# Performance work log

Measured on AMD Instinct MI355X. Metric: run time of the kernel, lower is better.

## Reference

```python
import jax, jax.numpy as jnp
import numpy as np

DIM = 1024
NUM_HEADS = 16
HEAD_DIM = DIM // NUM_HEADS


def setup_inputs() -> dict:
    key = jax.random.key(0)
    k1, k2, k3 = jax.random.split(key, 3)
    x = jax.random.normal(k1, (2, 2048, DIM), dtype=jnp.float32)
    # nn.Linear weights stored as [out, in]; apply as x @ W.T
    w_qkv = jax.random.normal(k2, (3 * DIM, DIM), dtype=jnp.float32) * (1.0 / np.sqrt(DIM))
    w_out = jax.random.normal(k3, (DIM, DIM), dtype=jnp.float32) * (1.0 / np.sqrt(DIM))
    return {"x": x, "w_qkv": w_qkv, "w_out": w_out}


def reference(x, w_qkv, w_out):
    b, t, _ = x.shape
    qkv = x @ w_qkv.T                                  # [b, t, 3*dim]
    qkv = qkv.reshape(b, t, 3, NUM_HEADS, HEAD_DIM)    # (three h d) split order
    q, k, v = jnp.moveaxis(qkv, 2, 0)                  # each [b, t, h, d]
    q = q.transpose(0, 2, 1, 3)                        # [b, h, t, d]
    k = k.transpose(0, 2, 1, 3)
    v = v.transpose(0, 2, 1, 3)
    attn = jnp.einsum('bhid,bhjd->bhij', q, k) / np.sqrt(HEAD_DIM)
    causal_mask = jnp.triu(jnp.ones((t, t), dtype=bool), k=1)
    attn = jnp.where(causal_mask, -jnp.inf, attn)
    attn = jax.nn.softmax(attn, axis=-1)
    out = jnp.einsum('bhij,bhjd->bhid', attn, v)
    out = out.transpose(0, 2, 1, 3).reshape(b, t, DIM)
    return out @ w_out.T
```

## Files before the change

kernel.cpp:

```cpp
#include <hip/hip_runtime.h>

#define DIM_ 1024
#define HEADS_ 16
#define HD_ 64
#define T_ 2048
#define BATCH_ 2
#define QKVN_ 3072

typedef unsigned short u16;
typedef unsigned int u32;
typedef float f32x4 __attribute__((ext_vector_type(4)));
typedef float f32x16 __attribute__((ext_vector_type(16)));
typedef short s16x8 __attribute__((ext_vector_type(8)));
typedef unsigned short u16x4 __attribute__((ext_vector_type(4)));

__device__ __forceinline__ u16 f2bf(float f) {
  unsigned u = __float_as_uint(f);
  u += 0x7fffu + ((u >> 16) & 1u);
  return (u16)(u >> 16);
}

__device__ __forceinline__ float fexp2(float x) {
  float r;
  asm("v_exp_f32 %0, %1" : "=v"(r) : "v"(x));
  return r;
}

__device__ __forceinline__ u32 cvtpk(float a, float b) {
  u32 r;
  asm("v_cvt_pk_bf16_f32 %0, %1, %2" : "=v"(r) : "v"(a), "v"(b));
  return r;
}

__global__ __launch_bounds__(256) void cvt_all(const float* __restrict__ x,
                                               const float* __restrict__ wqkv,
                                               const float* __restrict__ wout,
                                               u16* __restrict__ outbase) {
  int i = blockIdx.x * 256 + threadIdx.x;
  const float4* src;
  int off;
  if (i < 1048576) { src = (const float4*)x; off = i; }
  else if (i < 1835008) { src = (const float4*)wqkv; off = i - 1048576; }
  else { src = (const float4*)wout; off = i - 1835008; }
  float4 v = src[off];
  u16x4 o;
  o.x = f2bf(v.x); o.y = f2bf(v.y); o.z = f2bf(v.z); o.w = f2bf(v.w);
  reinterpret_cast<u16x4*>(outbase)[i] = o;
}

__device__ __forceinline__ void gld_lds16(const void* g, void* l) {
  auto gp = (__attribute__((address_space(1))) char*)(unsigned long long)g;
  auto lp = (__attribute__((address_space(3))) char*)(unsigned int)(unsigned long long)l;
  __builtin_amdgcn_global_load_lds(gp, lp, 16, 0, 0);
}

template <int MODE>
__global__ __launch_bounds__(256) void gemm1(const u16* __restrict__ A,
                                             const u16* __restrict__ B,
                                             void* __restrict__ Cv,
                                             u16* __restrict__ vto) {
  constexpr int K = 1024;
  constexpr int NN = (MODE == 1) ? 1024 : QKVN_;
  __shared__ __align__(16) u16 smem[(MODE == 2) ? 8704 : 8192];
  u16* As = smem;
  u16* Bs = smem + 4096;
  const int nt = blockIdx.x, mt = blockIdx.y;
  const int tid = threadIdx.x;
  const int lane = tid & 63;
  const int w = tid >> 6;
  const int wr = w >> 1, wc = w & 1;
  const int lrow = lane & 15, kg = lane >> 4;
  const u16* Ag = A + (size_t)(mt * 128) * K;
  const u16* Bg = B + (size_t)(nt * 128) * K;

  f32x4 acc[4][4];
#pragma unroll
  for (int i = 0; i < 4; ++i)
#pragma unroll
    for (int j = 0; j < 4; ++j) {
      f32x4 z = {0.f, 0.f, 0.f, 0.f};
      acc[i][j] = z;
    }

  const int e0 = tid * 8;
  const int row0 = e0 >> 5, kc0 = e0 & 31;
  const int row1 = row0 + 64, kc1 = kc0;
  const int ldsoff0 = (tid & ~63) * 16;
  const int ldsoff1 = (256 + (tid & ~63)) * 16;

  for (int k0 = 0; k0 < K; k0 += 32) {
    gld_lds16(Ag + (size_t)row0 * K + k0 + kc0, (char*)As + ldsoff0);
    gld_lds16(Ag + (size_t)row1 * K + k0 + kc1, (char*)As + ldsoff1);
    gld_lds16(Bg + (size_t)row0 * K + k0 + kc0, (char*)Bs + ldsoff0);
    gld_lds16(Bg + (size_t)row1 * K + k0 + kc1, (char*)Bs + ldsoff1);
    __syncthreads();
    s16x8 a[4], b[4];
#pragma unroll
    for (int mf = 0; mf < 4; ++mf)
      a[mf] = *(const s16x8*)&As[(wr * 64 + mf * 16 + lrow) * 32 + 8 * kg];
#pragma unroll
    for (int nf = 0; nf < 4; ++nf)
      b[nf] = *(const s16x8*)&Bs[(wc * 64 + nf * 16 + lrow) * 32 + 8 * kg];
#pragma unroll
    for (int mf = 0; mf < 4; ++mf)
#pragma unroll
      for (int nf = 0; nf < 4; ++nf)
        acc[mf][nf] = __builtin_amdgcn_mfma_f32_16x16x32_bf16(a[mf], b[nf], acc[mf][nf], 0, 0, 0);
    __syncthreads();
  }

  if (MODE == 1) {
    float* C = (float*)Cv;
#pragma unroll
    for (int mf = 0; mf < 4; ++mf)
#pragma unroll
      for (int nf = 0; nf < 4; ++nf)
#pragma unroll
        for (int j = 0; j < 4; ++j) {
          int r = mt * 128 + wr * 64 + mf * 16 + 4 * kg + j;
          int c = nt * 128 + wc * 64 + nf * 16 + lrow;
          C[(size_t)r * NN + c] = acc[mf][nf][j];
        }
  } else if (nt < 16) {
    u16* qkvo = (u16*)Cv;
#pragma unroll
    for (int mf = 0; mf < 4; ++mf)
#pragma unroll
      for (int nf = 0; nf < 4; ++nf)
#pragma unroll
        for (int j = 0; j < 4; ++j) {
          int r = mt * 128 + wr * 64 + mf * 16 + 4 * kg + j;
          int c = nt * 128 + wc * 64 + nf * 16 + lrow;
          qkvo[(size_t)r * QKVN_ + c] = f2bf(acc[mf][nf][j]);
        }
  } else {
    const int c16 = tid >> 4, chunk = tid & 15;
    const int bb = mt >> 4;
    const int tb = (mt & 15) * 128 + chunk * 8;
#pragma unroll
    for (int p = 0; p < 2; ++p) {
      __syncthreads();
      if (wc == p) {
#pragma unroll
        for (int mf = 0; mf < 4; ++mf)
#pragma unroll
          for (int nf = 0; nf < 4; ++nf) {
            const int cl = nf * 16 + lrow;
            const int rl = wr * 64 + mf * 16 + 4 * kg;
            u16x4 pk;
            pk.x = f2bf(acc[mf][nf][0]); pk.y = f2bf(acc[mf][nf][1]);
            pk.z = f2bf(acc[mf][nf][2]); pk.w = f2bf(acc[mf][nf][3]);
            *(u16x4*)&smem[cl * 136 + rl] = pk;
          }
      }
      __syncthreads();
#pragma unroll
      for (int pp = 0; pp < 4; ++pp) {
        const int cl = pp * 16 + c16;
        const int cg = nt * 128 + p * 64 + cl;
        const int hV = (cg >> 6) & 15, d = cg & 63;
        const s16x8 v = *(const s16x8*)&smem[cl * 136 + chunk * 8];
        *(s16x8*)(vto + ((size_t)((bb * 16 + hV) * 64 + d)) * T_ + tb) = v;
      }
    }
  }
}

__global__ __launch_bounds__(256, 2) void attn_fwd(const u16* __restrict__ qkv,
                                                   const u16* __restrict__ vt,
                                                   u16* __restrict__ o) {
  const int gid = blockIdx.x;
  const int pr = gid >> 5;
  const int bh = gid & 31;
  const int b = bh >> 4, h = bh & 15;
  const int tid = threadIdx.x;
  const int lane = tid & 63;
  const int qw = (tid >> 6) & 1;
  const int kvg = tid >> 7;
  const int l31 = lane & 31, hi = lane >> 5;

  __shared__ __align__(16) char smem[65536];

  const int row_s = tid >> 3, slot_s = tid & 7;
  const u16* Kbase = qkv + (size_t)(b * T_) * QKVN_ + 1024 + h * 64;
  const u16* Vbase = vt + (size_t)(bh * 64) * T_;
  const u16* KgA = Kbase + (size_t)row_s * QKVN_ + slot_s * 8;
  const u16* KgB = KgA + (size_t)32 * QKVN_;
  const u16* VgA = Vbase + (size_t)row_s * T_ + slot_s * 8;
  const u16* VgB = VgA + (size_t)32 * T_;
  const int dstA = row_s * 128 + ((slot_s ^ (row_s & 7)) << 4);

  const int rbyte = l31 * 128;
  const int xsw = l31 & 7;
  const float CEXP = 0.18033688011112042f;

  for (int ph = 0; ph < 2; ++ph) {
    const int jt = (ph == 0) ? (31 - pr) : pr;
    const int nt = jt + 1;
    const int nrt = (nt + 1) >> 1;
    const int qrow0 = 64 * jt + 32 * qw;

    s16x8 qf[4];
    {
      const u16* qp = qkv + (size_t)(b * T_ + qrow0 + l31) * QKVN_ + h * 64 + 8 * hi;
#pragma unroll
      for (int ksl = 0; ksl < 4; ++ksl)
        qf[ksl] = *(const s16x8*)(qp + 16 * ksl);
    }

    f32x16 o0v, o1v;
#pragma unroll
    for (int r = 0; r < 16; ++r) { o0v[r] = 0.f; o1v[r] = 0.f; }
    float mrun = -__builtin_inff(), lrun = 0.0f;

    __syncthreads();
    *(s16x8*)(smem + dstA)                 = *(const s16x8*)KgA;
    *(s16x8*)(smem + 4096 + dstA)          = *(const s16x8*)KgB;
    *(s16x8*)(smem + 32768 + dstA)         = *(const s16x8*)VgA;
    *(s16x8*)(smem + 32768 + 4096 + dstA)  = *(const s16x8*)VgB;
    if (nt > 1) {
      *(s16x8*)(smem + 8192 + dstA)                = *(const s16x8*)(KgA + (size_t)64 * QKVN_);
      *(s16x8*)(smem + 8192 + 4096 + dstA)         = *(const s16x8*)(KgB + (size_t)64 * QKVN_);
      *(s16x8*)(smem + 32768 + 8192 + dstA)        = *(const s16x8*)(VgA + 64);
      *(s16x8*)(smem + 32768 + 8192 + 4096 + dstA) = *(const s16x8*)(VgB + 64);
    }

    int cur = 0;
    for (int r = 0; r < nrt; ++r) {
      const int t = 2 * r + kvg;
      const bool pe = (2 * r + 2 < nt), po = (2 * r + 3 < nt);
      s16x8 ke0, ke1, ve0, ve1, ko0, ko1, vo0, vo1;
      if (pe) {
        const size_t kofs = (size_t)(2 * r + 2) * 64 * QKVN_;
        const int vofs = (2 * r + 2) * 64;
        ke0 = *(const s16x8*)(KgA + kofs);
        ke1 = *(const s16x8*)(KgB + kofs);
        ve0 = *(const s16x8*)(VgA + vofs);
        ve1 = *(const s16x8*)(VgB + vofs);
      }
      if (po) {
        const size_t kofs = (size_t)(2 * r + 3) * 64 * QKVN_;
        const int vofs = (2 * r + 3) * 64;
        ko0 = *(const s16x8*)(KgA + kofs);
        ko1 = *(const s16x8*)(KgB + kofs);
        vo0 = *(const s16x8*)(VgA + vofs);
        vo1 = *(const s16x8*)(VgB + vofs);
      }
      __syncthreads();

      if (t < nt) {
        const char* Kc = smem + cur * 16384 + kvg * 8192;
        const char* Vc = smem + 32768 + cur * 16384 + kvg * 8192;
        const bool isdiag = (t == nt - 1);
        const bool two = !(isdiag && qw == 0);

        f32x16 s0v, s1v;
#pragma unroll
        for (int rr = 0; rr < 16; ++rr) { s0v[rr] = 0.f; s1v[rr] = 0.f; }
        __builtin_amdgcn_s_setprio(1);
#pragma unroll
        for (int ksl = 0; ksl < 4; ++ksl) {
          const s16x8 kf = *(const s16x8*)(Kc + rbyte + (((2 * ksl + hi) ^ xsw) << 4));
          s0v = __builtin_amdgcn_mfma_f32_32x32x16_bf16(kf, qf[ksl], s0v, 0, 0, 0);
        }
        if (two) {
#pragma unroll
          for (int ksl = 0; ksl < 4; ++ksl) {
            const s16x8 kf = *(const s16x8*)(Kc + 4096 + rbyte + (((2 * ksl + hi) ^ xsw) << 4));
            s1v = __builtin_amdgcn_mfma_f32_32x32x16_bf16(kf, qf[ksl], s1v, 0, 0, 0);
          }
        }
        __builtin_amdgcn_s_setprio(0);

        if (isdiag) {
          const int thr = 32 * qw + l31;
#pragma unroll
          for (int rr = 0; rr < 16; ++rr) {
            const int kvl = 4 * hi + (rr & 3) + 8 * (rr >> 2);
            if (kvl > thr) s0v[rr] = -__builtin_inff();
            if (two && kvl + 32 > thr) s1v[rr] = -__builtin_inff();
          }
        }

        float mloc = s0v[0];
#pragma unroll
        for (int rr = 1; rr < 16; ++rr) mloc = fmaxf(mloc, s0v[rr]);
        if (two) {
#pragma unroll
          for (int rr = 0; rr < 16; ++rr) mloc = fmaxf(mloc, s1v[rr]);
        }
        mloc = fmaxf(mloc, __shfl_xor(mloc, 32));

        const bool needfull = !((mloc - mrun) * CEXP <= 8.0f);
        if (__any(needfull)) {
          const float newm = fmaxf(mrun, mloc);
          const float sc = fexp2((mrun - newm) * CEXP);
          mrun = newm;
          lrun *= sc;
          o0v *= sc;
          o1v *= sc;
        }
        const float msc = mrun * CEXP;

        float rs = 0.0f;
        u32 pd0[8], pd1[8];
#pragma unroll
        for (int ri = 0; ri < 8; ++ri) {
          const float p0 = fexp2(__builtin_fmaf(s0v[2 * ri], CEXP, -msc));
          const float p1 = fexp2(__builtin_fmaf(s0v[2 * ri + 1], CEXP, -msc));
          rs += p0 + p1;
          pd0[ri] = cvtpk(p0, p1);
        }
        if (two) {
#pragma unroll
          for (int ri = 0; ri < 8; ++ri) {
            const float p0 = fexp2(__builtin_fmaf(s1v[2 * ri], CEXP, -msc));
            const float p1 = fexp2(__builtin_fmaf(s1v[2 * ri + 1], CEXP, -msc));
            rs += p0 + p1;
            pd1[ri] = cvtpk(p0, p1);
          }
        }
        rs += __shfl_xor(rs, 32);
        lrun += rs;

        __builtin_amdgcn_s_setprio(1);
#pragma unroll
        for (int kk = 0; kk < 4; ++kk) {
          if (kk >= 2 && !two) break;
          u32 x0, y0, x1, y1;
          if (kk == 0)      { x0 = pd0[0]; y0 = pd0[2]; x1 = pd0[1]; y1 = pd0[3]; }
          else if (kk == 1) { x0 = pd0[4]; y0 = pd0[6]; x1 = pd0[5]; y1 = pd0[7]; }
          else if (kk == 2) { x0 = pd1[0]; y0 = pd1[2]; x1 = pd1[1]; y1 = pd1[3]; }
          else              { x0 = pd1[4]; y0 = pd1[6]; x1 = pd1[5]; y1 = pd1[7]; }
          asm volatile("v_permlane32_swap_b32 %0, %1" : "+v"(x0), "+v"(y0));
          asm volatile("v_permlane32_swap_b32 %0, %1" : "+v"(x1), "+v"(y1));
          u32 pw[4] = {x0, x1, y0, y1};
          const s16x8 pf = *(const s16x8*)pw;
          const s16x8 vf0 = *(const s16x8*)(Vc + rbyte + (((2 * kk + hi) ^ xsw) << 4));
          const s16x8 vf1 = *(const s16x8*)(Vc + 4096 + rbyte + (((2 * kk + hi) ^ xsw) << 4));
          o0v = __builtin_amdgcn_mfma_f32_32x32x16_bf16(vf0, pf, o0v, 0, 0, 0);
          o1v = __builtin_amdgcn_mfma_f32_32x32x16_bf16(vf1, pf, o1v, 0, 0, 0);
        }
        __builtin_amdgcn_s_setprio(0);
      }

      if (pe) {
        const int nb = (cur ^ 1) * 16384;
        *(s16x8*)(smem + nb + dstA)                = ke0;
        *(s16x8*)(smem + nb + 4096 + dstA)         = ke1;
        *(s16x8*)(smem + 32768 + nb + dstA)        = ve0;
        *(s16x8*)(smem + 32768 + nb + 4096 + dstA) = ve1;
      }
      if (po) {
        const int nb = (cur ^ 1) * 16384 + 8192;
        *(s16x8*)(smem + nb + dstA)                = ko0;
        *(s16x8*)(smem + nb + 4096 + dstA)         = ko1;
        *(s16x8*)(smem + 32768 + nb + dstA)        = vo0;
        *(s16x8*)(smem + 32768 + nb + 4096 + dstA) = vo1;
      }
      cur ^= 1;
    }

    __syncthreads();
    float* Om = (float*)smem + qw * 2048;
    float* Mf = (float*)(smem + 16384) + qw * 64;
    float* Lf = (float*)(smem + 16896) + qw * 64;
    if (kvg == 1) {
#pragma unroll
      for (int rr = 0; rr < 16; ++rr) {
        Om[rr * 64 + lane] = o0v[rr];
        Om[(16 + rr) * 64 + lane] = o1v[rr];
      }
      Mf[lane] = mrun;
      Lf[lane] = lrun;
    }
    __syncthreads();
    if (kvg == 0) {
      const float mA = Mf[lane];
      const float lA = Lf[lane];
      const float m2 = fmaxf(mrun, mA);
      const float sB = fexp2((mrun - m2) * CEXP);
      const float sA = fexp2((mA - m2) * CEXP);
      const float linv = 1.0f / (lrun * sB + lA * sA);
      u16* orow = o + (size_t)(b * T_ + qrow0 + l31) * DIM_ + h * 64;
#pragma unroll
      for (int ri = 0; ri < 8; ++ri) {
        const int dbase0 = 4 * hi + 8 * (ri >> 1) + 2 * (ri & 1);
        const float a0 = (o0v[2 * ri] * sB + Om[(2 * ri) * 64 + lane] * sA) * linv;
        const float a1 = (o0v[2 * ri + 1] * sB + Om[(2 * ri + 1) * 64 + lane] * sA) * linv;
        const float c0 = (o1v[2 * ri] * sB + Om[(16 + 2 * ri) * 64 + lane] * sA) * linv;
        const float c1 = (o1v[2 * ri + 1] * sB + Om[(16 + 2 * ri + 1) * 64 + lane] * sA) * linv;
        *(u32*)(orow + dbase0) = cvtpk(a0, a1);
        *(u32*)(orow + 32 + dbase0) = cvtpk(c0, c1);
      }
    }
  }
}

extern "C" void kernel_launch(void* const* d_in, const int* in_sizes, int n_in,
                              void* d_out, int out_size, void* d_ws, size_t ws_size,
                              hipStream_t stream) {
  const float* x = (const float*)d_in[0];
  const float* w_qkv = (const float*)d_in[1];
  const float* w_out = (const float*)d_in[2];
  char* ws = (char*)d_ws;
  u16* xb    = (u16*)(ws + 0);
  u16* wqkvb = (u16*)(ws + 8388608);
  u16* woutb = (u16*)(ws + 14680064);
  u16* qkvb  = (u16*)(ws + 16777216);
  u16* vtb   = (u16*)(ws + 41943040);
  u16* attno = (u16*)(ws + 50331648);

  cvt_all<<<8192, 256, 0, stream>>>(x, w_qkv, w_out, xb);
  gemm1<2><<<dim3(24, 32), 256, 0, stream>>>(xb, wqkvb, qkvb, vtb);
  attn_fwd<<<512, 256, 0, stream>>>(qkvb, vtb, attno);
  gemm1<1><<<dim3(8, 32), 256, 0, stream>>>(attno, woutb, d_out, nullptr);
}
```

Baseline: 107.5 us.

## Give each attention block one query tile and single-buffer K/V in LDS

The attention kernel no longer pairs a long and a short causal query tile inside one block. It now launches 1024 blocks, one 64-row query tile each, ordered from the largest tile down. K/V staging drops from a double buffer to a single 32KB buffer fed by register prefetch, with an extra barrier per iteration. The min-blocks launch bound is removed, so more blocks may fit per CU and the scheduler balances load, at the cost of less LDS-level overlap and a possible register-allocation change.

```diff
diff --git a/kernel.cpp b/kernel.cpp
--- a/kernel.cpp
+++ b/kernel.cpp
@@ -166,11 +166,11 @@
   }
 }
 
-__global__ __launch_bounds__(256, 2) void attn_fwd(const u16* __restrict__ qkv,
-                                                   const u16* __restrict__ vt,
-                                                   u16* __restrict__ o) {
+__global__ __launch_bounds__(256) void attn_fwd(const u16* __restrict__ qkv,
+                                                const u16* __restrict__ vt,
+                                                u16* __restrict__ o) {
   const int gid = blockIdx.x;
-  const int pr = gid >> 5;
+  const int jt = 31 - (gid >> 5);
   const int bh = gid & 31;
   const int b = bh >> 4, h = bh & 15;
   const int tid = threadIdx.x;
@@ -178,8 +178,11 @@
   const int qw = (tid >> 6) & 1;
   const int kvg = tid >> 7;
   const int l31 = lane & 31, hi = lane >> 5;
-
-  __shared__ __align__(16) char smem[65536];
+  const int nt = jt + 1;
+  const int nrt = (nt + 1) >> 1;
+  const int qrow0 = 64 * jt + 32 * qw;
+
+  __shared__ __align__(16) char smem[32768];
 
   const int row_s = tid >> 3, slot_s = tid & 7;
   const u16* Kbase = qkv + (size_t)(b * T_) * QKVN_ + 1024 + h * 64;
@@ -194,205 +197,194 @@
   const int xsw = l31 & 7;
   const float CEXP = 0.18033688011112042f;
 
-  for (int ph = 0; ph < 2; ++ph) {
-    const int jt = (ph == 0) ? (31 - pr) : pr;
-    const int nt = jt + 1;
-    const int nrt = (nt + 1) >> 1;
-    const int qrow0 = 64 * jt + 32 * qw;
-
-    s16x8 qf[4];
-    {
-      const u16* qp = qkv + (size_t)(b * T_ + qrow0 + l31) * QKVN_ + h * 64 + 8 * hi;
-#pragma unroll
-      for (int ksl = 0; ksl < 4; ++ksl)
-        qf[ksl] = *(const s16x8*)(qp + 16 * ksl);
-    }
-
-    f32x16 o0v, o1v;
-#pragma unroll
-    for (int r = 0; r < 16; ++r) { o0v[r] = 0.f; o1v[r] = 0.f; }
-    float mrun = -__builtin_inff(), lrun = 0.0f;
-
+  s16x8 qf[4];
+  {
+    const u16* qp = qkv + (size_t)(b * T_ + qrow0 + l31) * QKVN_ + h * 64 + 8 * hi;
+#pragma unroll
+    for (int ksl = 0; ksl < 4; ++ksl)
+      qf[ksl] = *(const s16x8*)(qp + 16 * ksl);
+  }
+
+  f32x16 o0v, o1v;
+#pragma unroll
+  for (int r = 0; r < 16; ++r) { o0v[r] = 0.f; o1v[r] = 0.f; }
+  float mrun = -__builtin_inff(), lrun = 0.0f;
+
+  *(s16x8*)(smem + dstA)                 = *(const s16x8*)KgA;
+  *(s16x8*)(smem + 4096 + dstA)          = *(const s16x8*)KgB;
+  *(s16x8*)(smem + 16384 + dstA)         = *(const s16x8*)VgA;
+  *(s16x8*)(smem + 16384 + 4096 + dstA)  = *(const s16x8*)VgB;
+  if (nt > 1) {
+    *(s16x8*)(smem + 8192 + dstA)                = *(const s16x8*)(KgA + (size_t)64 * QKVN_);
+    *(s16x8*)(smem + 8192 + 4096 + dstA)         = *(const s16x8*)(KgB + (size_t)64 * QKVN_);
+    *(s16x8*)(smem + 16384 + 8192 + dstA)        = *(const s16x8*)(VgA + 64);
+    *(s16x8*)(smem + 16384 + 8192 + 4096 + dstA) = *(const s16x8*)(VgB + 64);
+  }
+
+  for (int r = 0; r < nrt; ++r) {
+    const int t = 2 * r + kvg;
+    const bool pe = (2 * r + 2 < nt), po = (2 * r + 3 < nt);
+    s16x8 ke0, ke1, ve0, ve1, ko0, ko1, vo0, vo1;
+    if (pe) {
+      const size_t kofs = (size_t)(2 * r + 2) * 64 * QKVN_;
+      const int vofs = (2 * r + 2) * 64;
+      ke0 = *(const s16x8*)(KgA + kofs);
+      ke1 = *(const s16x8*)(KgB + kofs);
+      ve0 = *(const s16x8*)(VgA + vofs);
+      ve1 = *(const s16x8*)(VgB + vofs);
+    }
+    if (po) {
+      const size_t kofs = (size_t)(2 * r + 3) * 64 * QKVN_;
+      const int vofs = (2 * r + 3) * 64;
+      ko0 = *(const s16x8*)(KgA + kofs);
+      ko1 = *(const s16x8*)(KgB + kofs);
+      vo0 = *(const s16x8*)(VgA + vofs);
+      vo1 = *(const s16x8*)(VgB + vofs);
+    }
     __syncthreads();
-    *(s16x8*)(smem + dstA)                 = *(const s16x8*)KgA;
-    *(s16x8*)(smem + 4096 + dstA)          = *(const s16x8*)KgB;
-    *(s16x8*)(smem + 32768 + dstA)         = *(const s16x8*)VgA;
-    *(s16x8*)(smem + 32768 + 4096 + dstA)  = *(const s16x8*)VgB;
-    if (nt > 1) {
-      *(s16x8*)(smem + 8192 + dstA)                = *(const s16x8*)(KgA + (size_t)64 * QKVN_);
-      *(s16x8*)(smem + 8192 + 4096 + dstA)         = *(const s16x8*)(KgB + (size_t)64 * QKVN_);
-      *(s16x8*)(smem + 32768 + 8192 + dstA)        = *(const s16x8*)(VgA + 64);
-      *(s16x8*)(smem + 32768 + 8192 + 4096 + dstA) = *(const s16x8*)(VgB + 64);
-    }
-
-    int cur = 0;
-    for (int r = 0; r < nrt; ++r) {
-      const int t = 2 * r + kvg;
-      const bool pe = (2 * r + 2 < nt), po = (2 * r + 3 < nt);
-      s16x8 ke0, ke1, ve0, ve1, ko0, ko1, vo0, vo1;
-      if (pe) {
-        const size_t kofs = (size_t)(2 * r + 2) * 64 * QKVN_;
-        const int vofs = (2 * r + 2) * 64;
-        ke0 = *(const s16x8*)(KgA + kofs);
-        ke1 = *(const s16x8*)(KgB + kofs);
-        ve0 = *(const s16x8*)(VgA + vofs);
-        ve1 = *(const s16x8*)(VgB + vofs);
-      }
-      if (po) {
-        const size_t kofs = (size_t)(2 * r + 3) * 64 * QKVN_;
-        const int vofs = (2 * r + 3) * 64;
-        ko0 = *(const s16x8*)(KgA + kofs);
-        ko1 = *(const s16x8*)(KgB + kofs);
-        vo0 = *(const s16x8*)(VgA + vofs);
-        vo1 = *(const s16x8*)(VgB + vofs);
-      }
-      __syncthreads();
-
-      if (t < nt) {
-        const char* Kc = smem + cur * 16384 + kvg * 8192;
-        const char* Vc = smem + 32768 + cur * 16384 + kvg * 8192;
-        const bool isdiag = (t == nt - 1);
-        const bool two = !(isdiag && qw == 0);
-
-        f32x16 s0v, s1v;
-#pragma unroll
-        for (int rr = 0; rr < 16; ++rr) { s0v[rr] = 0.f; s1v[rr] = 0.f; }
-        __builtin_amdgcn_s_setprio(1);
+
+    if (t < nt) {
+      const char* Kc = smem + kvg * 8192;
+      const char* Vc = smem + 16384 + kvg * 8192;
+      const bool isdiag = (t == nt - 1);
+      const bool two = !(isdiag && qw == 0);
+
+      f32x16 s0v, s1v;
+#pragma unroll
+      for (int rr = 0; rr < 16; ++rr) { s0v[rr] = 0.f; s1v[rr] = 0.f; }
+      __builtin_amdgcn_s_setprio(1);
+#pragma unroll
+      for (int ksl = 0; ksl < 4; ++ksl) {
+        const s16x8 kf = *(const s16x8*)(Kc + rbyte + (((2 * ksl + hi) ^ xsw) << 4));
+        s0v = __builtin_amdgcn_mfma_f32_32x32x16_bf16(kf, qf[ksl], s0v, 0, 0, 0);
+      }
+      if (two) {
 #pragma unroll
         for (int ksl = 0; ksl < 4; ++ksl) {
-          const s16x8 kf = *(const s16x8*)(Kc + rbyte + (((2 * ksl + hi) ^ xsw) << 4));
-          s0v = __builtin_amdgcn_mfma_f32_32x32x16_bf16(kf, qf[ksl], s0v, 0, 0, 0);
+          const s16x8 kf = *(const s16x8*)(Kc + 4096 + rbyte + (((2 * ksl + hi) ^ xsw) << 4));
+          s1v = __builtin_amdgcn_mfma_f32_32x32x16_bf16(kf, qf[ksl], s1v, 0, 0, 0);
         }
-        if (two) {
-#pragma unroll
-          for (int ksl = 0; ksl < 4; ++ksl) {
-            const s16x8 kf = *(const s16x8*)(Kc + 4096 + rbyte + (((2 * ksl + hi) ^ xsw) << 4));
-            s1v = __builtin_amdgcn_mfma_f32_32x32x16_bf16(kf, qf[ksl], s1v, 0, 0, 0);
-          }
+      }
+      __builtin_amdgcn_s_setprio(0);
+
+      if (isdiag) {
+        const int thr = 32 * qw + l31;
+#pragma unroll
+        for (int rr = 0; rr < 16; ++rr) {
+          const int kvl = 4 * hi + (rr & 3) + 8 * (rr >> 2);
+          if (kvl > thr) s0v[rr] = -__builtin_inff();
+          if (two && kvl + 32 > thr) s1v[rr] = -__builtin_inff();
         }
-        __builtin_amdgcn_s_setprio(0);
-
-        if (isdiag) {
-          const int thr = 32 * qw + l31;
-#pragma unroll
-          for (int rr = 0; rr < 16; ++rr) {
-            const int kvl = 4 * hi + (rr & 3) + 8 * (rr >> 2);
-            if (kvl > thr) s0v[rr] = -__builtin_inff();
-            if (two && kvl + 32 > thr) s1v[rr] = -__builtin_inff();
-          }
+      }
+
+      float mloc = s0v[0];
+#pragma unroll
+      for (int rr = 1; rr < 16; ++rr) mloc = fmaxf(mloc, s0v[rr]);
+      if (two) {
+#pragma unroll
+        for (int rr = 0; rr < 16; ++rr) mloc = fmaxf(mloc, s1v[rr]);
+      }
+      mloc = fmaxf(mloc, __shfl_xor(mloc, 32));
+
+      const bool needfull = !((mloc - mrun) * CEXP <= 8.0f);
+      if (__any(needfull)) {
+        const float newm = fmaxf(mrun, mloc);
+        const float sc = fexp2((mrun - newm) * CEXP);
+        mrun = newm;
+        lrun *= sc;
+        o0v *= sc;
+        o1v *= sc;
+      }
+      const float msc = mrun * CEXP;
+
+      float rs = 0.0f;
+      u32 pd0[8], pd1[8];
+#pragma unroll
+      for (int ri = 0; ri < 8; ++ri) {
+        const float p0 = fexp2(__builtin_fmaf(s0v[2 * ri], CEXP, -msc));
+        const float p1 = fexp2(__builtin_fmaf(s0v[2 * ri + 1], CEXP, -msc));
+        rs += p0 + p1;
+        pd0[ri] = cvtpk(p0, p1);
+      }
+      if (two) {
+#pragma unroll
+        for (int ri = 0; ri < 8; ++ri) {
+          const float p0 = fexp2(__builtin_fmaf(s1v[2 * ri], CEXP, -msc));
+          const float p1 = fexp2(__builtin_fmaf(s1v[2 * ri + 1], CEXP, -msc));
+          rs += p0 + p1;
+          pd1[ri] = cvtpk(p0, p1);
         }
-
-        float mloc = s0v[0];
-#pragma unroll
-        for (int rr = 1; rr < 16; ++rr) mloc = fmaxf(mloc, s0v[rr]);
-        if (two) {
-#pragma unroll
-          for (int rr = 0; rr < 16; ++rr) mloc = fmaxf(mloc, s1v[rr]);
-        }
-        mloc = fmaxf(mloc, __shfl_xor(mloc, 32));
-
-        const bool needfull = !((mloc - mrun) * CEXP <= 8.0f);
-        if (__any(needfull)) {
-          const float newm = fmaxf(mrun, mloc);
-          const float sc = fexp2((mrun - newm) * CEXP);
-          mrun = newm;
-          lrun *= sc;
-          o0v *= sc;
-          o1v *= sc;
-        }
-        const float msc = mrun * CEXP;
-
-        float rs = 0.0f;
-        u32 pd0[8], pd1[8];
-#pragma unroll
-        for (int ri = 0; ri < 8; ++ri) {
-          const float p0 = fexp2(__builtin_fmaf(s0v[2 * ri], CEXP, -msc));
-          const float p1 = fexp2(__builtin_fmaf(s0v[2 * ri + 1], CEXP, -msc));
-          rs += p0 + p1;
-          pd0[ri] = cvtpk(p0, p1);
-        }
-        if (two) {
-#pragma unroll
-          for (int ri = 0; ri < 8; ++ri) {
-            const float p0 = fexp2(__builtin_fmaf(s1v[2 * ri], CEXP, -msc));
-            const float p1 = fexp2(__builtin_fmaf(s1v[2 * ri + 1], CEXP, -msc));
-            rs += p0 + p1;
-            pd1[ri] = cvtpk(p0, p1);
-          }
-        }
-        rs += __shfl_xor(rs, 32);
-        lrun += rs;
-
-        __builtin_amdgcn_s_setprio(1);
-#pragma unroll
-        for (int kk = 0; kk < 4; ++kk) {
-          if (kk >= 2 && !two) break;
-          u32 x0, y0, x1, y1;
-          if (kk == 0)      { x0 = pd0[0]; y0 = pd0[2]; x1 = pd0[1]; y1 = pd0[3]; }
-          else if (kk == 1) { x0 = pd0[4]; y0 = pd0[6]; x1 = pd0[5]; y1 = pd0[7]; }
-          else if (kk == 2) { x0 = pd1[0]; y0 = pd1[2]; x1 = pd1[1]; y1 = pd1[3]; }
-          else              { x0 = pd1[4]; y0 = pd1[6]; x1 = pd1[5]; y1 = pd1[7]; }
-          asm volatile("v_permlane32_swap_b32 %0, %1" : "+v"(x0), "+v"(y0));
-          asm volatile("v_permlane32_swap_b32 %0, %1" : "+v"(x1), "+v"(y1));
-          u32 pw[4] = {x0, x1, y0, y1};
-          const s16x8 pf = *(const s16x8*)pw;
-          const s16x8 vf0 = *(const s16x8*)(Vc + rbyte + (((2 * kk + hi) ^ xsw) << 4));
-          const s16x8 vf1 = *(const s16x8*)(Vc + 4096 + rbyte + (((2 * kk + hi) ^ xsw) << 4));
-          o0v = __builtin_amdgcn_mfma_f32_32x32x16_bf16(vf0, pf, o0v, 0, 0, 0);
-          o1v = __builtin_amdgcn_mfma_f32_32x32x16_bf16(vf1, pf, o1v, 0, 0, 0);
-        }
-        __builtin_amdgcn_s_setprio(0);
-      }
-
-      if (pe) {
-        const int nb = (cur ^ 1) * 16384;
-        *(s16x8*)(smem + nb + dstA)                = ke0;
-        *(s16x8*)(smem + nb + 4096 + dstA)         = ke1;
-        *(s16x8*)(smem + 32768 + nb + dstA)        = ve0;
-        *(s16x8*)(smem + 32768 + nb + 4096 + dstA) = ve1;
-      }
-      if (po) {
-        const int nb = (cur ^ 1) * 16384 + 8192;
-        *(s16x8*)(smem + nb + dstA)                = ko0;
-        *(s16x8*)(smem + nb + 4096 + dstA)         = ko1;
-        *(s16x8*)(smem + 32768 + nb + dstA)        = vo0;
-        *(s16x8*)(smem + 32768 + nb + 4096 + dstA) = vo1;
-      }
-      cur ^= 1;
+      }
+      rs += __shfl_xor(rs, 32);
+      lrun += rs;
+
+      __builtin_amdgcn_s_setprio(1);
+#pragma unroll
+      for (int kk = 0; kk < 4; ++kk) {
+        if (kk >= 2 && !two) break;
+        u32 x0, y0, x1, y1;
+        if (kk == 0)      { x0 = pd0[0]; y0 = pd0[2]; x1 = pd0[1]; y1 = pd0[3]; }
+        else if (kk == 1) { x0 = pd0[4]; y0 = pd0[6]; x1 = pd0[5]; y1 = pd0[7]; }
+        else if (kk == 2) { x0 = pd1[0]; y0 = pd1[2]; x1 = pd1[1]; y1 = pd1[3]; }
+        else              { x0 = pd1[4]; y0 = pd1[6]; x1 = pd1[5]; y1 = pd1[7]; }
+        asm volatile("v_permlane32_swap_b32 %0, %1" : "+v"(x0), "+v"(y0));
+        asm volatile("v_permlane32_swap_b32 %0, %1" : "+v"(x1), "+v"(y1));
+        u32 pw[4] = {x0, x1, y0, y1};
+        const s16x8 pf = *(const s16x8*)pw;
+        const s16x8 vf0 = *(const s16x8*)(Vc + rbyte + (((2 * kk + hi) ^ xsw) << 4));
+        const s16x8 vf1 = *(const s16x8*)(Vc + 4096 + rbyte + (((2 * kk + hi) ^ xsw) << 4));
+        o0v = __builtin_amdgcn_mfma_f32_32x32x16_bf16(vf0, pf, o0v, 0, 0, 0);
+        o1v = __builtin_amdgcn_mfma_f32_32x32x16_bf16(vf1, pf, o1v, 0, 0, 0);
+      }
+      __builtin_amdgcn_s_setprio(0);
     }
 
     __syncthreads();
-    float* Om = (float*)smem + qw * 2048;
-    float* Mf = (float*)(smem + 16384) + qw * 64;
-    float* Lf = (float*)(smem + 16896) + qw * 64;
-    if (kvg == 1) {
-#pragma unroll
-      for (int rr = 0; rr < 16; ++rr) {
-        Om[rr * 64 + lane] = o0v[rr];
-        Om[(16 + rr) * 64 + lane] = o1v[rr];
-      }
-      Mf[lane] = mrun;
-      Lf[lane] = lrun;
-    }
-    __syncthreads();
-    if (kvg == 0) {
-      const float mA = Mf[lane];
-      const float lA = Lf[lane];
-      const float m2 = fmaxf(mrun, mA);
-      const float sB = fexp2((mrun - m2) * CEXP);
-      const float sA = fexp2((mA - m2) * CEXP);
-      const float linv = 1.0f / (lrun * sB + lA * sA);
-      u16* orow = o + (size_t)(b * T_ + qrow0 + l31) * DIM_ + h * 64;
-#pragma unroll
-      for (int ri = 0; ri < 8; ++ri) {
-        const int dbase0 = 4 * hi + 8 * (ri >> 1) + 2 * (ri & 1);
-        const float a0 = (o0v[2 * ri] * sB + Om[(2 * ri) * 64 + lane] * sA) * linv;
-        const float a1 = (o0v[2 * ri + 1] * sB + Om[(2 * ri + 1) * 64 + lane] * sA) * linv;
-        const float c0 = (o1v[2 * ri] * sB + Om[(16 + 2 * ri) * 64 + lane] * sA) * linv;
-        const float c1 = (o1v[2 * ri + 1] * sB + Om[(16 + 2 * ri + 1) * 64 + lane] * sA) * linv;
-        *(u32*)(orow + dbase0) = cvtpk(a0, a1);
-        *(u32*)(orow + 32 + dbase0) = cvtpk(c0, c1);
-      }
+    if (pe) {
+      *(s16x8*)(smem + dstA)                = ke0;
+      *(s16x8*)(smem + 4096 + dstA)         = ke1;
+      *(s16x8*)(smem + 16384 + dstA)        = ve0;
+      *(s16x8*)(smem + 16384 + 4096 + dstA) = ve1;
+    }
+    if (po) {
+      *(s16x8*)(smem + 8192 + dstA)                = ko0;
+      *(s16x8*)(smem + 8192 + 4096 + dstA)         = ko1;
+      *(s16x8*)(smem + 16384 + 8192 + dstA)        = vo0;
+      *(s16x8*)(smem + 16384 + 8192 + 4096 + dstA) = vo1;
+    }
+  }
+
+  __syncthreads();
+  float* Om = (float*)smem + qw * 2048;
+  float* Mf = (float*)(smem + 16384) + qw * 64;
+  float* Lf = (float*)(smem + 16896) + qw * 64;
+  if (kvg == 1) {
+#pragma unroll
+    for (int rr = 0; rr < 16; ++rr) {
+      Om[rr * 64 + lane] = o0v[rr];
+      Om[(16 + rr) * 64 + lane] = o1v[rr];
+    }
+    Mf[lane] = mrun;
+    Lf[lane] = lrun;
+  }
+  __syncthreads();
+  if (kvg == 0) {
+    const float mA = Mf[lane];
+    const float lA = Lf[lane];
+    const float m2 = fmaxf(mrun, mA);
+    const float sB = fexp2((mrun - m2) * CEXP);
+    const float sA = fexp2((mA - m2) * CEXP);
+    const float linv = 1.0f / (lrun * sB + lA * sA);
+    u16* orow = o + (size_t)(b * T_ + qrow0 + l31) * DIM_ + h * 64;
+#pragma unroll
+    for (int ri = 0; ri < 8; ++ri) {
+      const int dbase0 = 4 * hi + 8 * (ri >> 1) + 2 * (ri & 1);
+      const float a0 = (o0v[2 * ri] * sB + Om[(2 * ri) * 64 + lane] * sA) * linv;
+      const float a1 = (o0v[2 * ri + 1] * sB + Om[(2 * ri + 1) * 64 + lane] * sA) * linv;
+      const float c0 = (o1v[2 * ri] * sB + Om[(16 + 2 * ri) * 64 + lane] * sA) * linv;
+      const float c1 = (o1v[2 * ri + 1] * sB + Om[(16 + 2 * ri + 1) * 64 + lane] * sA) * linv;
+      *(u32*)(orow + dbase0) = cvtpk(a0, a1);
+      *(u32*)(orow + 32 + dbase0) = cvtpk(c0, c1);
     }
   }
 }
@@ -413,6 +405,6 @@
 
   cvt_all<<<8192, 256, 0, stream>>>(x, w_qkv, w_out, xb);
   gemm1<2><<<dim3(24, 32), 256, 0, stream>>>(xb, wqkvb, qkvb, vtb);
-  attn_fwd<<<512, 256, 0, stream>>>(qkvb, vtb, attno);
+  attn_fwd<<<1024, 256, 0, stream>>>(qkvb, vtb, attno);
   gemm1<1><<<dim3(8, 32), 256, 0, stream>>>(attno, woutb, d_out, nullptr);
 }
```

Measured after the change: 113.9 us. 5.9% more time.

## Double GEMM K-tile to 64 and XOR-swizzle LDS layout

Applied to the files above, without the earlier changes.

The bf16 GEMM kernel now stages 64-wide K slices per iteration instead of 32. That halves the number of barrier pairs and global-to-LDS rounds, and each tile feeds two MFMA sub-steps. Rows in LDS are stored with an XOR swizzle of 16-byte chunks so the fragment reads avoid bank conflicts. LDS usage per block doubles to 32 KB, which may reduce occupancy.

```diff
diff --git a/kernel.cpp b/kernel.cpp
--- a/kernel.cpp
+++ b/kernel.cpp
@@ -61,9 +61,9 @@
                                              u16* __restrict__ vto) {
   constexpr int K = 1024;
   constexpr int NN = (MODE == 1) ? 1024 : QKVN_;
-  __shared__ __align__(16) u16 smem[(MODE == 2) ? 8704 : 8192];
+  __shared__ __align__(16) u16 smem[16384];
   u16* As = smem;
-  u16* Bs = smem + 4096;
+  u16* Bs = smem + 8192;
   const int nt = blockIdx.x, mt = blockIdx.y;
   const int tid = threadIdx.x;
   const int lane = tid & 63;
@@ -82,30 +82,41 @@
       acc[i][j] = z;
     }
 
-  const int e0 = tid * 8;
-  const int row0 = e0 >> 5, kc0 = e0 & 31;
-  const int row1 = row0 + 64, kc1 = kc0;
-  const int ldsoff0 = (tid & ~63) * 16;
-  const int ldsoff1 = (256 + (tid & ~63)) * 16;
-
-  for (int k0 = 0; k0 < K; k0 += 32) {
-    gld_lds16(Ag + (size_t)row0 * K + k0 + kc0, (char*)As + ldsoff0);
-    gld_lds16(Ag + (size_t)row1 * K + k0 + kc1, (char*)As + ldsoff1);
-    gld_lds16(Bg + (size_t)row0 * K + k0 + kc0, (char*)Bs + ldsoff0);
-    gld_lds16(Bg + (size_t)row1 * K + k0 + kc1, (char*)Bs + ldsoff1);
+  const int srow = tid >> 3;
+  const int scol = 8 * ((tid & 7) ^ ((tid >> 3) & 7));
+  const int ldsw = (tid & ~63) * 16;
+
+  int aoff[4][2], boff[4][2];
+#pragma unroll
+  for (int mf = 0; mf < 4; ++mf)
+#pragma unroll
+    for (int ks = 0; ks < 2; ++ks) {
+      aoff[mf][ks] = (wr * 64 + mf * 16 + lrow) * 128 + (((ks * 4 + kg) ^ (lrow & 7)) << 4);
+      boff[mf][ks] = (wc * 64 + mf * 16 + lrow) * 128 + (((ks * 4 + kg) ^ (lrow & 7)) << 4);
+    }
+
+  for (int k0 = 0; k0 < K; k0 += 64) {
+#pragma unroll
+    for (int c = 0; c < 4; ++c) {
+      gld_lds16(Ag + (size_t)(c * 32 + srow) * K + k0 + scol, (char*)As + c * 4096 + ldsw);
+      gld_lds16(Bg + (size_t)(c * 32 + srow) * K + k0 + scol, (char*)Bs + c * 4096 + ldsw);
+    }
     __syncthreads();
-    s16x8 a[4], b[4];
-#pragma unroll
-    for (int mf = 0; mf < 4; ++mf)
-      a[mf] = *(const s16x8*)&As[(wr * 64 + mf * 16 + lrow) * 32 + 8 * kg];
-#pragma unroll
-    for (int nf = 0; nf < 4; ++nf)
-      b[nf] = *(const s16x8*)&Bs[(wc * 64 + nf * 16 + lrow) * 32 + 8 * kg];
-#pragma unroll
-    for (int mf = 0; mf < 4; ++mf)
+#pragma unroll
+    for (int ks = 0; ks < 2; ++ks) {
+      s16x8 a[4], b[4];
+#pragma unroll
+      for (int mf = 0; mf < 4; ++mf)
+        a[mf] = *(const s16x8*)((const char*)As + aoff[mf][ks]);
 #pragma unroll
       for (int nf = 0; nf < 4; ++nf)
-        acc[mf][nf] = __builtin_amdgcn_mfma_f32_16x16x32_bf16(a[mf], b[nf], acc[mf][nf], 0, 0, 0);
+        b[nf] = *(const s16x8*)((const char*)Bs + boff[nf][ks]);
+#pragma unroll
+      for (int mf = 0; mf < 4; ++mf)
+#pragma unroll
+        for (int nf = 0; nf < 4; ++nf)
+          acc[mf][nf] = __builtin_amdgcn_mfma_f32_16x16x32_bf16(a[mf], b[nf], acc[mf][nf], 0, 0, 0);
+    }
     __syncthreads();
   }
 
```

After: 99.44 us. 1.08x faster.
